# Performance work log

Hardware: AMD Instinct MI355X
Metric: run time of the kernel (lower is better)

The kernel has to match this reference:

```python
import jax, jax.numpy as jnp
import numpy as np

N = 100000   # nodes
E = 400000   # edges
B = 4000     # graphs
D = 300      # emb_dim
L = 5        # num_layer
MAX_LEN = 50 # max_atom_num (hard-coded in forward)
SELF_LOOP_BOND_TYPE = 4
BN_EPS = 1e-5


def setup_inputs() -> dict:
    key = jax.random.key(0)
    ks = jax.random.split(key, 12)
    x = jax.random.randint(ks[0], (N, 2), 0, 3)            # col0 atom type (<120), col1 chirality (<3)
    edge_index = jax.random.randint(ks[1], (2, E), 0, N)
    edge_attr = jax.random.randint(ks[2], (E, 2), 0, 3)    # col0 bond type (<6), col1 direction (<3)
    batch = jnp.sort(jax.random.randint(ks[3], (N,), 0, B))
    sc = 0.05
    x_emb1 = jax.random.normal(ks[4], (120, D)) * sc
    x_emb2 = jax.random.normal(ks[5], (3, D)) * sc
    e_emb1 = jax.random.normal(ks[6], (L, 6, D)) * sc
    e_emb2 = jax.random.normal(ks[7], (L, 3, D)) * sc
    W1 = jax.random.normal(ks[8], (L, D, 2 * D)) * (1.0 / np.sqrt(D))
    b1 = jnp.zeros((L, 2 * D))
    W2 = jax.random.normal(ks[9], (L, 2 * D, D)) * (1.0 / np.sqrt(2 * D))
    b2 = jnp.zeros((L, D))
    bn_gamma = jnp.ones((L, D))
    bn_beta = jnp.zeros((L, D))
    return dict(x=x, edge_index=edge_index, edge_attr=edge_attr, batch=batch,
                num_graphs=B, x_emb1=x_emb1, x_emb2=x_emb2, e_emb1=e_emb1,
                e_emb2=e_emb2, W1=W1, b1=b1, W2=W2, b2=b2,
                bn_gamma=bn_gamma, bn_beta=bn_beta)


def reference(x, edge_index, edge_attr, batch, num_graphs,
              x_emb1, x_emb2, e_emb1, e_emb2, W1, b1, W2, b2, bn_gamma, bn_beta):
    n = x.shape[0]
    # input node embedding: atom type + chirality
    h = x_emb1[x[:, 0]] + x_emb2[x[:, 1]]  # [N, D]
    # add self loops (bond_type=4, direction=0)
    loop = jnp.arange(n)
    src = jnp.concatenate([edge_index[0], loop])
    dst = jnp.concatenate([edge_index[1], loop])
    ea0 = jnp.concatenate([edge_attr[:, 0], jnp.full((n,), SELF_LOOP_BOND_TYPE, edge_attr.dtype)])
    ea1 = jnp.concatenate([edge_attr[:, 1], jnp.zeros((n,), edge_attr.dtype)])
    num_layers = W1.shape[0]
    for l in range(num_layers):
        ee = e_emb1[l][ea0] + e_emb2[l][ea1]                 # [E+N, D] edge embeddings
        msg = h[src] + ee                                     # gather + message
        agg = jax.ops.segment_sum(msg, dst, num_segments=n)   # scatter-add aggregation
        hid = jax.nn.relu(agg @ W1[l] + b1[l])                # GIN MLP
        h2 = hid @ W2[l] + b2[l]
        mean = h2.mean(axis=0)                                # BatchNorm1d (batch stats, biased var)
        var = jnp.mean((h2 - mean) ** 2, axis=0)
        h2 = (h2 - mean) * jax.lax.rsqrt(var + BN_EPS) * bn_gamma[l] + bn_beta[l]
        # dropout with drop_ratio=0 is identity; relu on all but last layer
        h = h2 if l == num_layers - 1 else jax.nn.relu(h2)
    # global mean pool over graphs
    counts = jax.ops.segment_sum(jnp.ones((n,), h.dtype), batch, num_segments=num_graphs)
    pooled = jax.ops.segment_sum(h, batch, num_segments=num_graphs) / jnp.maximum(counts, 1.0)[:, None]
    # atom_feature_pad: pad per-graph node features to MAX_LEN with mask
    idx = jnp.arange(n)
    is_start = jnp.concatenate([jnp.array([True]), batch[1:] != batch[:-1]])
    start = jax.lax.cummax(jnp.where(is_start, idx, 0))
    pos = idx - start                                          # position within each graph
    valid = pos < MAX_LEN
    posc = jnp.minimum(pos, MAX_LEN - 1)
    d = h.shape[1]
    node_feature = jnp.zeros((num_graphs, MAX_LEN, d), h.dtype).at[batch, posc].add(
        h * valid[:, None].astype(h.dtype))
    mask = jnp.zeros((num_graphs, MAX_LEN), h.dtype).at[batch, posc].add(valid.astype(h.dtype))
    return pooled, node_feature, mask
```

## Files before the change

### kernel.cpp

```cpp
#include <hip/hip_runtime.h>
#include <cstdint>

#define D 300
#define MAXLEN 50
#define K1P 320
#define H1 600
#define H1P 608
#define W1ROWS 640
#define W2ROWS 384

typedef __attribute__((ext_vector_type(8))) short s16x8;
typedef __attribute__((ext_vector_type(4))) short s16x4;
typedef __attribute__((ext_vector_type(4))) float f32x4;
typedef __attribute__((ext_vector_type(2))) float f32x2;
typedef __attribute__((ext_vector_type(4))) int i32x4;

__device__ __forceinline__ unsigned short f2b(float f) {
  uint32_t u = __builtin_bit_cast(uint32_t, f);
  u += 0x7FFFu + ((u >> 16) & 1u);
  return (unsigned short)(u >> 16);
}
__device__ __forceinline__ float b2f(unsigned short s) {
  return __builtin_bit_cast(float, (uint32_t)s << 16);
}
__device__ __forceinline__ void gld_lds16(const void* g, void* l) {
  __builtin_amdgcn_global_load_lds((const __attribute__((address_space(1))) void*)g,
                                   (__attribute__((address_space(3))) void*)l, 16, 0, 0);
}

__global__ void k_cmb(const float* __restrict__ xe1, const float* __restrict__ xe2,
                      unsigned short* __restrict__ cmb, int total ) {
  int i = blockIdx.x * blockDim.x + threadIdx.x;
  if (i >= total) return;
  int c = i / 75, d = (i - c * 75) * 4;
  int a = c / 3, b = c - a * 3;
  s16x4 out;
#pragma unroll
  for (int j = 0; j < 4; ++j) out[j] = (short)f2b(xe1[(size_t)a * D + d + j] + xe2[(size_t)b * D + d + j]);
  *(s16x4*)(cmb + (size_t)c * K1P + d) = out;
}

__global__ void k_cid(const int* __restrict__ x, int* __restrict__ cid, int N) {
  int i = blockIdx.x * blockDim.x + threadIdx.x;
  if (i < N) cid[i] = x[2 * i] * 3 + x[2 * i + 1];
}

__global__ void k_padfill(unsigned short* __restrict__ aggbf, int N) {
  int idx = blockIdx.x * blockDim.x + threadIdx.x;
  if (idx >= N * 10) return;
  int i = idx / 10, j = idx - i * 10;
  *(uint32_t*)(aggbf + (size_t)i * K1P + D + j * 2) = 0;
}

__global__ void k_count(const int* __restrict__ key, int* __restrict__ cnt, int n) {
  int i = blockIdx.x * blockDim.x + threadIdx.x;
  if (i < n) atomicAdd(&cnt[key[i]], 1);
}

__global__ void k_scan1(const int* __restrict__ in, int* __restrict__ part, int n) {
  __shared__ int red[256];
  int tid = threadIdx.x;
  int base = blockIdx.x * 1024 + tid * 4;
  i32x4 v = {0, 0, 0, 0};
  if (base + 3 < n) v = *(const i32x4*)(in + base);
  else {
#pragma unroll
    for (int k = 0; k < 4; ++k) v[k] = (base + k < n) ? in[base + k] : 0;
  }
  int s = v[0] + v[1] + v[2] + v[3];
  red[tid] = s;
  __syncthreads();
  for (int off = 1; off < 256; off <<= 1) {
    int t = (tid >= off) ? red[tid - off] : 0;
    __syncthreads();
    red[tid] += t;
    __syncthreads();
  }
  if (tid == 255) part[blockIdx.x] = red[255];
}

__global__ void k_scan2(int* __restrict__ part, int P) {
  __shared__ int sm[1024];
  int tid = threadIdx.x;
  int v = (tid < P) ? part[tid] : 0;
  sm[tid] = v;
  __syncthreads();
  for (int off = 1; off < 1024; off <<= 1) {
    int t = (tid >= off) ? sm[tid - off] : 0;
    __syncthreads();
    sm[tid] += t;
    __syncthreads();
  }
  if (tid < P) part[tid] = sm[tid] - v;
  if (tid == 1023) part[P] = sm[1023];
}

__global__ void k_scan3(const int* __restrict__ in, const int* __restrict__ part,
                        int* __restrict__ out, int n, int P) {
  __shared__ int red[256];
  int tid = threadIdx.x;
  int base = blockIdx.x * 1024 + tid * 4;
  i32x4 v = {0, 0, 0, 0};
  if (base + 3 < n) v = *(const i32x4*)(in + base);
  else {
#pragma unroll
    for (int k = 0; k < 4; ++k) v[k] = (base + k < n) ? in[base + k] : 0;
  }
  int s = v[0] + v[1] + v[2] + v[3];
  red[tid] = s;
  __syncthreads();
  for (int off = 1; off < 256; off <<= 1) {
    int t = (tid >= off) ? red[tid - off] : 0;
    __syncthreads();
    red[tid] += t;
    __syncthreads();
  }
  int pre = red[tid] - s + part[blockIdx.x];
  if (base < n) out[base] = pre;
  if (base + 1 < n) out[base + 1] = pre + v[0];
  if (base + 2 < n) out[base + 2] = pre + v[0] + v[1];
  if (base + 3 < n) out[base + 3] = pre + v[0] + v[1] + v[2];
  if (blockIdx.x == 0 && tid == 0) out[n] = part[P];
}

__global__ void k_fill(const int* __restrict__ src, const int* __restrict__ dst,
                       const int* __restrict__ ea, const int* __restrict__ cid,
                       int* __restrict__ cur, const int* __restrict__ offs,
                       int* __restrict__ ssrc, int* __restrict__ seco,
                       int* __restrict__ scid, int E_) {
  int e = blockIdx.x * blockDim.x + threadIdx.x;
  if (e >= E_) return;
  int d = dst[e];
  int s = src[e];
  int p = atomicAdd(&cur[d], 1);
  int pos = offs[d] + p;
  ssrc[pos] = s;
  seco[pos] = ea[2 * e] * 3 + ea[2 * e + 1];
  scid[pos] = cid[s];
}

__global__ void k_ecomb(const float* __restrict__ e1, const float* __restrict__ e2,
                        float* __restrict__ ec, int total) {
  int i = blockIdx.x * blockDim.x + threadIdx.x;
  if (i >= total) return;
  int d = i % D;
  int c = (i / D) % 18;
  int l = i / (18 * D);
  int c0 = c / 3, c1 = c - c0 * 3;
  ec[i] = e1[((size_t)l * 6 + c0) * D + d] + e2[((size_t)l * 3 + c1) * D + d];
}

template <int FUSE>
__global__ void k_agg(const unsigned short* __restrict__ hin, const int* __restrict__ ridx,
                      const int* __restrict__ seco, const int* __restrict__ offs,
                      const float* __restrict__ ec, const float* __restrict__ scale,
                      const float* __restrict__ shift, const int* __restrict__ selfcid,
                      unsigned short* __restrict__ aggbf, int N) {
  int w = (int)((blockIdx.x * blockDim.x + threadIdx.x) >> 6);
  if (w >= N) return;
  int lane = threadIdx.x & 63;
  float sc0[3], sc1[3], sh0[3], sh1[3];
#pragma unroll
  for (int i = 0; i < 3; ++i) {
    int d2 = i * 64 + lane;
    if (FUSE && d2 < 150) {
      f32x2 s = *(const f32x2*)(scale + d2 * 2);
      f32x2 t = *(const f32x2*)(shift + d2 * 2);
      sc0[i] = s[0]; sc1[i] = s[1]; sh0[i] = t[0]; sh1[i] = t[1];
    } else { sc0[i] = sc1[i] = sh0[i] = sh1[i] = 0.f; }
  }
  int beg = offs[w], end = offs[w + 1];
  int wrow = FUSE ? w : selfcid[w];
  float s0[3], s1[3];
#pragma unroll
  for (int i = 0; i < 3; ++i) {
    int d2 = i * 64 + lane;
    float a = 0.f, b = 0.f;
    if (d2 < 150) {
      uint32_t u = *(const uint32_t*)(hin + (size_t)wrow * K1P + d2 * 2);
      f32x2 e = *(const f32x2*)(ec + 12 * D + d2 * 2);
      a = b2f((unsigned short)(u & 0xFFFF));
      b = b2f((unsigned short)(u >> 16));
      if (FUSE) { a = fmaxf(a * sc0[i] + sh0[i], 0.f); b = fmaxf(b * sc1[i] + sh1[i], 0.f); }
      a += e[0]; b += e[1];
    }
    s0[i] = a; s1[i] = b;
  }
  int j = beg;
  for (; j + 4 <= end; j += 4) {
    int sv0 = ridx[j], sv1 = ridx[j + 1], sv2 = ridx[j + 2], sv3 = ridx[j + 3];
    int co0 = seco[j], co1 = seco[j + 1], co2 = seco[j + 2], co3 = seco[j + 3];
    const unsigned short* p0 = hin + (size_t)sv0 * K1P;
    const unsigned short* p1 = hin + (size_t)sv1 * K1P;
    const unsigned short* p2 = hin + (size_t)sv2 * K1P;
    const unsigned short* p3 = hin + (size_t)sv3 * K1P;
    const float* t0 = ec + (size_t)co0 * D;
    const float* t1 = ec + (size_t)co1 * D;
    const float* t2 = ec + (size_t)co2 * D;
    const float* t3 = ec + (size_t)co3 * D;
#pragma unroll
    for (int i = 0; i < 3; ++i) {
      int d2 = i * 64 + lane;
      if (d2 < 150) {
        uint32_t u0 = *(const uint32_t*)(p0 + d2 * 2);
        uint32_t u1 = *(const uint32_t*)(p1 + d2 * 2);
        uint32_t u2 = *(const uint32_t*)(p2 + d2 * 2);
        uint32_t u3 = *(const uint32_t*)(p3 + d2 * 2);
        f32x2 e0 = *(const f32x2*)(t0 + d2 * 2);
        f32x2 e1v = *(const f32x2*)(t1 + d2 * 2);
        f32x2 e2v = *(const f32x2*)(t2 + d2 * 2);
        f32x2 e3 = *(const f32x2*)(t3 + d2 * 2);
        float a0 = b2f((unsigned short)(u0 & 0xFFFF)), b0 = b2f((unsigned short)(u0 >> 16));
        float a1 = b2f((unsigned short)(u1 & 0xFFFF)), b1 = b2f((unsigned short)(u1 >> 16));
        float a2 = b2f((unsigned short)(u2 & 0xFFFF)), b2 = b2f((unsigned short)(u2 >> 16));
        float a3 = b2f((unsigned short)(u3 & 0xFFFF)), b3 = b2f((unsigned short)(u3 >> 16));
        if (FUSE) {
          a0 = fmaxf(a0 * sc0[i] + sh0[i], 0.f); b0 = fmaxf(b0 * sc1[i] + sh1[i], 0.f);
          a1 = fmaxf(a1 * sc0[i] + sh0[i], 0.f); b1 = fmaxf(b1 * sc1[i] + sh1[i], 0.f);
          a2 = fmaxf(a2 * sc0[i] + sh0[i], 0.f); b2 = fmaxf(b2 * sc1[i] + sh1[i], 0.f);
          a3 = fmaxf(a3 * sc0[i] + sh0[i], 0.f); b3 = fmaxf(b3 * sc1[i] + sh1[i], 0.f);
        }
        s0[i] += (a0 + e0[0]) + (a1 + e1v[0]) + (a2 + e2v[0]) + (a3 + e3[0]);
        s1[i] += (b0 + e0[1]) + (b1 + e1v[1]) + (b2 + e2v[1]) + (b3 + e3[1]);
      }
    }
  }
  for (; j < end; ++j) {
    int sv = ridx[j], co = seco[j];
    const unsigned short* rp = hin + (size_t)sv * K1P;
    const float* tp = ec + (size_t)co * D;
#pragma unroll
    for (int i = 0; i < 3; ++i) {
      int d2 = i * 64 + lane;
      if (d2 < 150) {
        uint32_t u = *(const uint32_t*)(rp + d2 * 2);
        f32x2 e = *(const f32x2*)(tp + d2 * 2);
        float a = b2f((unsigned short)(u & 0xFFFF)), b = b2f((unsigned short)(u >> 16));
        if (FUSE) { a = fmaxf(a * sc0[i] + sh0[i], 0.f); b = fmaxf(b * sc1[i] + sh1[i], 0.f); }
        s0[i] += a + e[0];
        s1[i] += b + e[1];
      }
    }
  }
#pragma unroll
  for (int i = 0; i < 3; ++i) {
    int d2 = i * 64 + lane;
    if (d2 < 150) {
      uint32_t o = (uint32_t)f2b(s0[i]) | ((uint32_t)f2b(s1[i]) << 16);
      *(uint32_t*)(aggbf + (size_t)w * K1P + d2 * 2) = o;
    }
  }
}

__global__ void k_wconv(const float* __restrict__ W, unsigned short* __restrict__ Wt,
                        int K, int Nout, int Kp, int total) {
  int idx = blockIdx.x * blockDim.x + threadIdx.x;
  if (idx >= total) return;
  int n = idx / Kp, k = idx - n * Kp;
  float v = (k < K && n < Nout) ? W[(size_t)k * Nout + n] : 0.f;
  Wt[idx] = f2b(v);
}

template <int K, int EPI>
__global__ __launch_bounds__(256, 3) void k_gemm(
    const unsigned short* __restrict__ A, const unsigned short* __restrict__ Bt,
    const float* __restrict__ bias, unsigned short* __restrict__ Cb,
    float* __restrict__ sums, int M, int Nout, int ldc, int CT) {
  constexpr int T = K / 32;
  __shared__ __align__(16) unsigned short smem[24576];

  int nwg = gridDim.x;
  int q = nwg >> 3, r8 = nwg & 7;
  int xcd = blockIdx.x & 7, oidx = blockIdx.x >> 3;
  int wid = (xcd < r8 ? xcd * (q + 1) : r8 * (q + 1) + (xcd - r8) * q) + oidx;
  int ct = wid % CT, rt = wid / CT;
  const int rowBase = rt * 128, colBase = ct * 128;

  const int tid = threadIdx.x, lane = tid & 63, wave = tid >> 6;
  const int wm = wave >> 1, wn = wave & 1;
  const int l15 = lane & 15, lg = lane >> 4;

  unsigned short* Asm = smem;
  unsigned short* Bsm = smem + 12288;

  auto stage = [&](int s, int t) {
#pragma unroll
    for (int i = 0; i < 2; ++i) {
      int u = tid + i * 256;
      int rr = u >> 2;
      int cdat = (u & 3) ^ ((rr >> 1) & 3);
      int gr = rowBase + rr; if (gr >= M) gr = M - 1;
      gld_lds16(A + (size_t)gr * K + t * 32 + cdat * 8, Asm + s * 4096 + u * 8);
      gld_lds16(Bt + (size_t)(colBase + rr) * K + t * 32 + cdat * 8, Bsm + s * 4096 + u * 8);
    }
  };

  f32x4 acc[4][4] = {};
  stage(0, 0);
  stage(1, 1);
#pragma unroll
  for (int t = 0; t < T; ++t) {
    if (t + 1 < T) asm volatile("s_waitcnt vmcnt(4)" ::: "memory");
    else           asm volatile("s_waitcnt vmcnt(0)" ::: "memory");
    __builtin_amdgcn_s_barrier();
    __builtin_amdgcn_sched_barrier(0);
    const unsigned short* bA = Asm + (t % 3) * 4096;
    const unsigned short* bB = Bsm + (t % 3) * 4096;
    s16x8 af[4], bf[4];
#pragma unroll
    for (int i = 0; i < 4; ++i) {
      int ra = wm * 64 + i * 16 + l15;
      int rb = wn * 64 + i * 16 + l15;
      af[i] = *(const s16x8*)(bA + ((size_t)ra * 4 + (lg ^ ((ra >> 1) & 3))) * 8);
      bf[i] = *(const s16x8*)(bB + ((size_t)rb * 4 + (lg ^ ((rb >> 1) & 3))) * 8);
    }
    if (t + 2 < T) stage((t + 2) % 3, t + 2);
#pragma unroll
    for (int mi = 0; mi < 4; ++mi)
#pragma unroll
      for (int ni = 0; ni < 4; ++ni)
        acc[mi][ni] = __builtin_amdgcn_mfma_f32_16x16x32_bf16(af[mi], bf[ni], acc[mi][ni], 0, 0, 0);
  }

  float bnS[4] = {0.f, 0.f, 0.f, 0.f}, bnQ[4] = {0.f, 0.f, 0.f, 0.f};
#pragma unroll
  for (int ni = 0; ni < 4; ++ni) {
    int col = colBase + wn * 64 + ni * 16 + l15;
    if (col >= ldc) continue;
    bool inN = col < Nout;
    float bv = inN ? bias[col] : 0.f;
#pragma unroll
    for (int mi = 0; mi < 4; ++mi) {
      int row0 = rowBase + wm * 64 + mi * 16 + lg * 4;
#pragma unroll
      for (int rr = 0; rr < 4; ++rr) {
        int row = row0 + rr;
        if (row < M) {
          float v = inN ? acc[mi][ni][rr] + bv : 0.f;
          if (EPI) v = fmaxf(v, 0.f);
          else if (inN) { bnS[ni] += v; bnQ[ni] += v * v; }
          Cb[(size_t)row * ldc + col] = f2b(v);
        }
      }
    }
  }
  if (!EPI) {
#pragma unroll
    for (int ni = 0; ni < 4; ++ni) {
      float cs = bnS[ni], cq = bnQ[ni];
      cs += __shfl_xor(cs, 16); cq += __shfl_xor(cq, 16);
      cs += __shfl_xor(cs, 32); cq += __shfl_xor(cq, 32);
      int col = colBase + wn * 64 + ni * 16 + l15;
      if (lg == 0 && col < Nout) {
        atomicAdd(&sums[col], cs);
        atomicAdd(&sums[D + col], cq);
      }
    }
  }
}

__global__ void k_bnfinal(const float* __restrict__ sums, const float* __restrict__ sumsq,
                          const float* __restrict__ gamma, const float* __restrict__ beta,
                          float* __restrict__ scale, float* __restrict__ shift, int N) {
  int c = threadIdx.x;
  if (c >= D) return;
  float inv = 1.f / (float)N;
  float mean = sums[c] * inv;
  float var = sumsq[c] * inv - mean * mean;
  if (var < 0.f) var = 0.f;
  float sc = gamma[c] * rsqrtf(var + 1e-5f);
  scale[c] = sc;
  shift[c] = beta[c] - mean * sc;
}

__global__ void k_pool(const unsigned short* __restrict__ hb, const float* __restrict__ scale,
                       const float* __restrict__ shift, const int* __restrict__ gs,
                       const int* __restrict__ gc, float* __restrict__ pooled, int total ) {
  int gid = blockIdx.x * blockDim.x + threadIdx.x;
  if (gid >= total) return;
  int g = gid / 75, c4 = (gid - g * 75) * 4;
  int start = gs[g], cnt = gc[g];
  f32x4 s = {0.f, 0.f, 0.f, 0.f};
  for (int i = 0; i < cnt; ++i) {
    s16x4 in = *(const s16x4*)(hb + (size_t)(start + i) * K1P + c4);
#pragma unroll
    for (int j = 0; j < 4; ++j) s[j] += b2f((unsigned short)in[j]);
  }
  f32x4 sc = *(const f32x4*)(scale + c4);
  f32x4 sh = *(const f32x4*)(shift + c4);
  float dv = (cnt > 0) ? (float)cnt : 1.f;
  f32x4 out;
#pragma unroll
  for (int j = 0; j < 4; ++j) out[j] = (s[j] * sc[j] + sh[j] * (float)cnt) / dv;
  *(f32x4*)(pooled + (size_t)g * D + c4) = out;
}

__global__ void k_nf(const unsigned short* __restrict__ hb, const float* __restrict__ scale,
                     const float* __restrict__ shift, const int* __restrict__ gs,
                     const int* __restrict__ gc, float* __restrict__ nf, float* __restrict__ mask) {
  int g = blockIdx.x;
  int start = gs[g], cnt = gc[g];
  int lim = cnt < MAXLEN ? cnt : MAXLEN;
  for (int idx = threadIdx.x; idx < MAXLEN * 75; idx += 256) {
    int p = idx / 75;
    int c4 = (idx - p * 75) * 4;
    f32x4 v = {0.f, 0.f, 0.f, 0.f};
    if (p < lim) {
      s16x4 in = *(const s16x4*)(hb + (size_t)(start + p) * K1P + c4);
      f32x4 sc = *(const f32x4*)(scale + c4);
      f32x4 sh = *(const f32x4*)(shift + c4);
#pragma unroll
      for (int j = 0; j < 4; ++j) v[j] = b2f((unsigned short)in[j]) * sc[j] + sh[j];
    }
    *(f32x4*)(nf + (size_t)g * (MAXLEN * D) + p * D + c4) = v;
  }
  if (threadIdx.x < MAXLEN) mask[(size_t)g * MAXLEN + threadIdx.x] = (threadIdx.x < lim) ? 1.f : 0.f;
}

extern "C" void kernel_launch(void* const* d_in, const int* in_sizes, int n_in,
                              void* d_out, int out_size, void* d_ws, size_t ws_size,
                              hipStream_t stream) {
  const int* x      = (const int*)d_in[0];
  const int* ei     = (const int*)d_in[1];
  const int* ea     = (const int*)d_in[2];
  const int* batch  = (const int*)d_in[3];
  const float* xe1  = (const float*)d_in[5];
  const float* xe2  = (const float*)d_in[6];
  const float* ee1  = (const float*)d_in[7];
  const float* ee2  = (const float*)d_in[8];
  const float* W1   = (const float*)d_in[9];
  const float* b1   = (const float*)d_in[10];
  const float* W2   = (const float*)d_in[11];
  const float* b2   = (const float*)d_in[12];
  const float* gamma = (const float*)d_in[13];
  const float* beta  = (const float*)d_in[14];

  const int N = in_sizes[0] / 2;
  const int E = in_sizes[1] / 2;
  const int L = in_sizes[9] / (D * 2 * D);
  const int B = out_size / (D + MAXLEN * D + MAXLEN);

  char* ws = (char*)d_ws;
  size_t off = 0;
  auto alloc = [&](size_t bytes) -> void* {
    void* p = ws + off;
    off += (bytes + 255) & ~(size_t)255;
    return p;
  };
  unsigned short* aggbf = (unsigned short*)alloc((size_t)N * K1P * 2);
  unsigned short* hb    = (unsigned short*)alloc((size_t)N * K1P * 2);
  unsigned short* hid   = (unsigned short*)alloc((size_t)N * H1P * 2);
  unsigned short* cmb   = (unsigned short*)alloc((size_t)360 * K1P * 2);
  unsigned short* W1tA = (unsigned short*)alloc((size_t)L * W1ROWS * K1P * 2);
  unsigned short* W2tA = (unsigned short*)alloc((size_t)L * W2ROWS * H1P * 2);
  float* ecomb = (float*)alloc((size_t)L * 18 * D * 4);
  int* cnt    = (int*)alloc((size_t)N * 4);
  int* cur    = (int*)alloc((size_t)N * 4);
  int* offs   = (int*)alloc((size_t)(N + 1) * 4);
  int* cid    = (int*)alloc((size_t)N * 4);
  int* ssrc   = (int*)alloc((size_t)E * 4);
  int* seco   = (int*)alloc((size_t)E * 4);
  int* scid   = (int*)alloc((size_t)E * 4);
  int* gc     = (int*)alloc((size_t)B * 4);
  int* gs     = (int*)alloc((size_t)(B + 1) * 4);
  int* part   = (int*)alloc(1024 * 4);
  float* sumsA = (float*)alloc((size_t)L * 2 * D * 4);
  float* scale = (float*)alloc(2 * D * 4);

  hipMemsetAsync(cnt, 0, (size_t)N * 4, stream);
  hipMemsetAsync(cur, 0, (size_t)N * 4, stream);
  hipMemsetAsync(gc, 0, (size_t)B * 4, stream);
  hipMemsetAsync(sumsA, 0, (size_t)L * 2 * D * 4, stream);

  k_cmb<<<(360 * 75 + 255) / 256, 256, 0, stream>>>(xe1, xe2, cmb, 360 * 75);
  k_cid<<<(N + 255) / 256, 256, 0, stream>>>(x, cid, N);
  k_padfill<<<(N * 10 + 255) / 256, 256, 0, stream>>>(aggbf, N);
  k_count<<<(E + 255) / 256, 256, 0, stream>>>(ei + E, cnt, E);
  {
    int P = (N + 1023) / 1024;
    k_scan1<<<P, 256, 0, stream>>>(cnt, part, N);
    k_scan2<<<1, 1024, 0, stream>>>(part, P);
    k_scan3<<<P, 256, 0, stream>>>(cnt, part, offs, N, P);
  }
  k_fill<<<(E + 255) / 256, 256, 0, stream>>>(ei, ei + E, ea, cid, cur, offs, ssrc, seco, scid, E);
  k_count<<<(N + 255) / 256, 256, 0, stream>>>(batch, gc, N);
  {
    int P = (B + 1023) / 1024;
    k_scan1<<<P, 256, 0, stream>>>(gc, part, B);
    k_scan2<<<1, 1024, 0, stream>>>(part, P);
    k_scan3<<<P, 256, 0, stream>>>(gc, part, gs, B, P);
  }
  k_ecomb<<<(L * 18 * D + 255) / 256, 256, 0, stream>>>(ee1, ee2, ecomb, L * 18 * D);
  for (int l = 0; l < L; ++l) {
    k_wconv<<<(W1ROWS * K1P + 255) / 256, 256, 0, stream>>>(
        W1 + (size_t)l * D * H1, W1tA + (size_t)l * W1ROWS * K1P, D, H1, K1P, W1ROWS * K1P);
    k_wconv<<<(W2ROWS * H1P + 255) / 256, 256, 0, stream>>>(
        W2 + (size_t)l * H1 * D, W2tA + (size_t)l * W2ROWS * H1P, H1, D, H1P, W2ROWS * H1P);
  }

  const int RT = (N + 127) / 128;
  for (int l = 0; l < L; ++l) {
    float* sums = sumsA + (size_t)l * 2 * D;
    if (l == 0)
      k_agg<0><<<(N + 3) / 4, 256, 0, stream>>>(cmb, scid, seco, offs,
          ecomb + (size_t)l * 18 * D, nullptr, nullptr, cid, aggbf, N);
    else
      k_agg<1><<<(N + 3) / 4, 256, 0, stream>>>(hb, ssrc, seco, offs,
          ecomb + (size_t)l * 18 * D, scale, scale + D, nullptr, aggbf, N);
    k_gemm<K1P, 1><<<5 * RT, 256, 0, stream>>>(
        aggbf, W1tA + (size_t)l * W1ROWS * K1P, b1 + (size_t)l * H1, hid, nullptr, N, H1, H1P, 5);
    k_gemm<H1P, 0><<<3 * RT, 256, 0, stream>>>(
        hid, W2tA + (size_t)l * W2ROWS * H1P, b2 + (size_t)l * D, hb, sums, N, D, K1P, 3);
    k_bnfinal<<<1, 320, 0, stream>>>(sums, sums + D, gamma + (size_t)l * D, beta + (size_t)l * D,
                                     scale, scale + D, N);
  }

  float* out = (float*)d_out;
  float* out_pooled = out;
  float* out_nf = out + (size_t)B * D;
  float* out_mask = out + (size_t)B * D + (size_t)B * MAXLEN * D;
  k_pool<<<(B * 75 + 255) / 256, 256, 0, stream>>>(hb, scale, scale + D, gs, gc, out_pooled, B * 75);
  k_nf<<<B, 256, 0, stream>>>(hb, scale, scale + D, gs, gc, out_nf, out_mask);
}
```

Before: 1.835 ms.

## Fold edge embeddings into GEMM via per-node edge-type counts in padded K columns

Replaces the per-edge gather of edge-embedding rows in the aggregation kernel with an algebraic rewrite. Each node stores counts of its 18 incoming edge types (self loop included) in the otherwise-zero K padding columns of the aggregate matrix. Those columns are multiplied by precomputed (edge embedding @ W1) rows placed into the W1 padding. This removes the fp32 edge-table loads and the seco index stream from every layer's gather, at the cost of an extra atomic count pass and a small precompute kernel. The counts and the precomputed products are rounded to bf16, which changes numerics.

```diff
diff --git a/kernel.cpp b/kernel.cpp
--- a/kernel.cpp
+++ b/kernel.cpp
@@ -43,13 +43,6 @@
 __global__ void k_cid(const int* __restrict__ x, int* __restrict__ cid, int N) {
   int i = blockIdx.x * blockDim.x + threadIdx.x;
   if (i < N) cid[i] = x[2 * i] * 3 + x[2 * i + 1];
-}
-
-__global__ void k_padfill(unsigned short* __restrict__ aggbf, int N) {
-  int idx = blockIdx.x * blockDim.x + threadIdx.x;
-  if (idx >= N * 10) return;
-  int i = idx / 10, j = idx - i * 10;
-  *(uint32_t*)(aggbf + (size_t)i * K1P + D + j * 2) = 0;
 }
 
 __global__ void k_count(const int* __restrict__ key, int* __restrict__ cnt, int n) {
@@ -126,8 +119,8 @@
 __global__ void k_fill(const int* __restrict__ src, const int* __restrict__ dst,
                        const int* __restrict__ ea, const int* __restrict__ cid,
                        int* __restrict__ cur, const int* __restrict__ offs,
-                       int* __restrict__ ssrc, int* __restrict__ seco,
-                       int* __restrict__ scid, int E_) {
+                       int* __restrict__ ssrc, int* __restrict__ scid,
+                       int* __restrict__ cnt18, int E_) {
   int e = blockIdx.x * blockDim.x + threadIdx.x;
   if (e >= E_) return;
   int d = dst[e];
@@ -135,25 +128,43 @@
   int p = atomicAdd(&cur[d], 1);
   int pos = offs[d] + p;
   ssrc[pos] = s;
-  seco[pos] = ea[2 * e] * 3 + ea[2 * e + 1];
   scid[pos] = cid[s];
-}
-
-__global__ void k_ecomb(const float* __restrict__ e1, const float* __restrict__ e2,
-                        float* __restrict__ ec, int total) {
-  int i = blockIdx.x * blockDim.x + threadIdx.x;
-  if (i >= total) return;
-  int d = i % D;
-  int c = (i / D) % 18;
-  int l = i / (18 * D);
-  int c0 = c / 3, c1 = c - c0 * 3;
-  ec[i] = e1[((size_t)l * 6 + c0) * D + d] + e2[((size_t)l * 3 + c1) * D + d];
+  int co = ea[2 * e] * 3 + ea[2 * e + 1];
+  atomicAdd(&cnt18[d * 18 + co], 1);
+}
+
+__global__ void k_cnt18bf(const int* __restrict__ cnt18, unsigned short* __restrict__ aggbf, int N) {
+  int idx = blockIdx.x * blockDim.x + threadIdx.x;
+  if (idx >= N * 10) return;
+  int i = idx / 10, j = idx - i * 10;
+  uint32_t o = 0;
+  if (j < 9) {
+    int c0 = cnt18[i * 18 + 2 * j] + (2 * j == 12 ? 1 : 0);
+    int c1 = cnt18[i * 18 + 2 * j + 1];
+    o = (uint32_t)f2b((float)c0) | ((uint32_t)f2b((float)c1) << 16);
+  }
+  *(uint32_t*)(aggbf + (size_t)i * K1P + D + j * 2) = o;
+}
+
+__global__ void k_ecw1(const float* __restrict__ ee1, const float* __restrict__ ee2,
+                       const float* __restrict__ W1, unsigned short* __restrict__ W1tA,
+                       int L_, int total ) {
+  int idx = blockIdx.x * blockDim.x + threadIdx.x;
+  if (idx >= total) return;
+  int k18 = idx % 18;
+  int n = (idx / 18) % H1;
+  int l = idx / (18 * H1);
+  const float* e1 = ee1 + ((size_t)l * 6 + k18 / 3) * D;
+  const float* e2 = ee2 + ((size_t)l * 3 + k18 % 3) * D;
+  const float* w = W1 + (size_t)l * D * H1 + n;
+  float s = 0.f;
+  for (int d = 0; d < D; ++d) s += (e1[d] + e2[d]) * w[(size_t)d * H1];
+  W1tA[(size_t)l * W1ROWS * K1P + (size_t)n * K1P + D + k18] = f2b(s);
 }
 
 template <int FUSE>
 __global__ void k_agg(const unsigned short* __restrict__ hin, const int* __restrict__ ridx,
-                      const int* __restrict__ seco, const int* __restrict__ offs,
-                      const float* __restrict__ ec, const float* __restrict__ scale,
+                      const int* __restrict__ offs, const float* __restrict__ scale,
                       const float* __restrict__ shift, const int* __restrict__ selfcid,
                       unsigned short* __restrict__ aggbf, int N) {
   int w = (int)((blockIdx.x * blockDim.x + threadIdx.x) >> 6);
@@ -178,26 +189,19 @@
     float a = 0.f, b = 0.f;
     if (d2 < 150) {
       uint32_t u = *(const uint32_t*)(hin + (size_t)wrow * K1P + d2 * 2);
-      f32x2 e = *(const f32x2*)(ec + 12 * D + d2 * 2);
       a = b2f((unsigned short)(u & 0xFFFF));
       b = b2f((unsigned short)(u >> 16));
       if (FUSE) { a = fmaxf(a * sc0[i] + sh0[i], 0.f); b = fmaxf(b * sc1[i] + sh1[i], 0.f); }
-      a += e[0]; b += e[1];
     }
     s0[i] = a; s1[i] = b;
   }
   int j = beg;
   for (; j + 4 <= end; j += 4) {
     int sv0 = ridx[j], sv1 = ridx[j + 1], sv2 = ridx[j + 2], sv3 = ridx[j + 3];
-    int co0 = seco[j], co1 = seco[j + 1], co2 = seco[j + 2], co3 = seco[j + 3];
     const unsigned short* p0 = hin + (size_t)sv0 * K1P;
     const unsigned short* p1 = hin + (size_t)sv1 * K1P;
     const unsigned short* p2 = hin + (size_t)sv2 * K1P;
     const unsigned short* p3 = hin + (size_t)sv3 * K1P;
-    const float* t0 = ec + (size_t)co0 * D;
-    const float* t1 = ec + (size_t)co1 * D;
-    const float* t2 = ec + (size_t)co2 * D;
-    const float* t3 = ec + (size_t)co3 * D;
 #pragma unroll
     for (int i = 0; i < 3; ++i) {
       int d2 = i * 64 + lane;
@@ -206,10 +210,6 @@
         uint32_t u1 = *(const uint32_t*)(p1 + d2 * 2);
         uint32_t u2 = *(const uint32_t*)(p2 + d2 * 2);
         uint32_t u3 = *(const uint32_t*)(p3 + d2 * 2);
-        f32x2 e0 = *(const f32x2*)(t0 + d2 * 2);
-        f32x2 e1v = *(const f32x2*)(t1 + d2 * 2);
-        f32x2 e2v = *(const f32x2*)(t2 + d2 * 2);
-        f32x2 e3 = *(const f32x2*)(t3 + d2 * 2);
         float a0 = b2f((unsigned short)(u0 & 0xFFFF)), b0 = b2f((unsigned short)(u0 >> 16));
         float a1 = b2f((unsigned short)(u1 & 0xFFFF)), b1 = b2f((unsigned short)(u1 >> 16));
         float a2 = b2f((unsigned short)(u2 & 0xFFFF)), b2 = b2f((unsigned short)(u2 >> 16));
@@ -220,25 +220,23 @@
           a2 = fmaxf(a2 * sc0[i] + sh0[i], 0.f); b2 = fmaxf(b2 * sc1[i] + sh1[i], 0.f);
           a3 = fmaxf(a3 * sc0[i] + sh0[i], 0.f); b3 = fmaxf(b3 * sc1[i] + sh1[i], 0.f);
         }
-        s0[i] += (a0 + e0[0]) + (a1 + e1v[0]) + (a2 + e2v[0]) + (a3 + e3[0]);
-        s1[i] += (b0 + e0[1]) + (b1 + e1v[1]) + (b2 + e2v[1]) + (b3 + e3[1]);
+        s0[i] += (a0 + a1) + (a2 + a3);
+        s1[i] += (b0 + b1) + (b2 + b3);
       }
     }
   }
   for (; j < end; ++j) {
-    int sv = ridx[j], co = seco[j];
+    int sv = ridx[j];
     const unsigned short* rp = hin + (size_t)sv * K1P;
-    const float* tp = ec + (size_t)co * D;
 #pragma unroll
     for (int i = 0; i < 3; ++i) {
       int d2 = i * 64 + lane;
       if (d2 < 150) {
         uint32_t u = *(const uint32_t*)(rp + d2 * 2);
-        f32x2 e = *(const f32x2*)(tp + d2 * 2);
         float a = b2f((unsigned short)(u & 0xFFFF)), b = b2f((unsigned short)(u >> 16));
         if (FUSE) { a = fmaxf(a * sc0[i] + sh0[i], 0.f); b = fmaxf(b * sc1[i] + sh1[i], 0.f); }
-        s0[i] += a + e[0];
-        s1[i] += b + e[1];
+        s0[i] += a;
+        s1[i] += b;
       }
     }
   }
@@ -453,13 +451,12 @@
   unsigned short* cmb   = (unsigned short*)alloc((size_t)360 * K1P * 2);
   unsigned short* W1tA = (unsigned short*)alloc((size_t)L * W1ROWS * K1P * 2);
   unsigned short* W2tA = (unsigned short*)alloc((size_t)L * W2ROWS * H1P * 2);
-  float* ecomb = (float*)alloc((size_t)L * 18 * D * 4);
   int* cnt    = (int*)alloc((size_t)N * 4);
   int* cur    = (int*)alloc((size_t)N * 4);
   int* offs   = (int*)alloc((size_t)(N + 1) * 4);
   int* cid    = (int*)alloc((size_t)N * 4);
+  int* cnt18  = (int*)alloc((size_t)N * 18 * 4);
   int* ssrc   = (int*)alloc((size_t)E * 4);
-  int* seco   = (int*)alloc((size_t)E * 4);
   int* scid   = (int*)alloc((size_t)E * 4);
   int* gc     = (int*)alloc((size_t)B * 4);
   int* gs     = (int*)alloc((size_t)(B + 1) * 4);
@@ -470,11 +467,11 @@
   hipMemsetAsync(cnt, 0, (size_t)N * 4, stream);
   hipMemsetAsync(cur, 0, (size_t)N * 4, stream);
   hipMemsetAsync(gc, 0, (size_t)B * 4, stream);
+  hipMemsetAsync(cnt18, 0, (size_t)N * 18 * 4, stream);
   hipMemsetAsync(sumsA, 0, (size_t)L * 2 * D * 4, stream);
 
   k_cmb<<<(360 * 75 + 255) / 256, 256, 0, stream>>>(xe1, xe2, cmb, 360 * 75);
   k_cid<<<(N + 255) / 256, 256, 0, stream>>>(x, cid, N);
-  k_padfill<<<(N * 10 + 255) / 256, 256, 0, stream>>>(aggbf, N);
   k_count<<<(E + 255) / 256, 256, 0, stream>>>(ei + E, cnt, E);
   {
     int P = (N + 1023) / 1024;
@@ -482,7 +479,8 @@
     k_scan2<<<1, 1024, 0, stream>>>(part, P);
     k_scan3<<<P, 256, 0, stream>>>(cnt, part, offs, N, P);
   }
-  k_fill<<<(E + 255) / 256, 256, 0, stream>>>(ei, ei + E, ea, cid, cur, offs, ssrc, seco, scid, E);
+  k_fill<<<(E + 255) / 256, 256, 0, stream>>>(ei, ei + E, ea, cid, cur, offs, ssrc, scid, cnt18, E);
+  k_cnt18bf<<<(N * 10 + 255) / 256, 256, 0, stream>>>(cnt18, aggbf, N);
   k_count<<<(N + 255) / 256, 256, 0, stream>>>(batch, gc, N);
   {
     int P = (B + 1023) / 1024;
@@ -490,23 +488,21 @@
     k_scan2<<<1, 1024, 0, stream>>>(part, P);
     k_scan3<<<P, 256, 0, stream>>>(gc, part, gs, B, P);
   }
-  k_ecomb<<<(L * 18 * D + 255) / 256, 256, 0, stream>>>(ee1, ee2, ecomb, L * 18 * D);
   for (int l = 0; l < L; ++l) {
     k_wconv<<<(W1ROWS * K1P + 255) / 256, 256, 0, stream>>>(
         W1 + (size_t)l * D * H1, W1tA + (size_t)l * W1ROWS * K1P, D, H1, K1P, W1ROWS * K1P);
     k_wconv<<<(W2ROWS * H1P + 255) / 256, 256, 0, stream>>>(
         W2 + (size_t)l * H1 * D, W2tA + (size_t)l * W2ROWS * H1P, H1, D, H1P, W2ROWS * H1P);
   }
+  k_ecw1<<<(L * H1 * 18 + 255) / 256, 256, 0, stream>>>(ee1, ee2, W1, W1tA, L, L * H1 * 18);
 
   const int RT = (N + 127) / 128;
   for (int l = 0; l < L; ++l) {
     float* sums = sumsA + (size_t)l * 2 * D;
     if (l == 0)
-      k_agg<0><<<(N + 3) / 4, 256, 0, stream>>>(cmb, scid, seco, offs,
-          ecomb + (size_t)l * 18 * D, nullptr, nullptr, cid, aggbf, N);
+      k_agg<0><<<(N + 3) / 4, 256, 0, stream>>>(cmb, scid, offs, nullptr, nullptr, cid, aggbf, N);
     else
-      k_agg<1><<<(N + 3) / 4, 256, 0, stream>>>(hb, ssrc, seco, offs,
-          ecomb + (size_t)l * 18 * D, scale, scale + D, nullptr, aggbf, N);
+      k_agg<1><<<(N + 3) / 4, 256, 0, stream>>>(hb, ssrc, offs, scale, scale + D, nullptr, aggbf, N);
     k_gemm<K1P, 1><<<5 * RT, 256, 0, stream>>>(
         aggbf, W1tA + (size_t)l * W1ROWS * K1P, b1 + (size_t)l * H1, hid, nullptr, N, H1, H1P, 5);
     k_gemm<H1P, 0><<<3 * RT, 256, 0, stream>>>(
```

Measured after the change: 1.667 ms. 1.1x faster.
